# Performance work log

Hardware: AMD Instinct MI355X
Metric: run time of the kernel (lower is better)

## Reference

```python
import jax, jax.numpy as jnp
import numpy as np

V, J, NB = 6890, 52, 16
NPOSE = (J - 1) * 9  # 459 pose-blendshape features
# Standard SMPL-H kinematic tree: 22 body joints + left hand (wrist 20) + right hand (wrist 21)
PARENTS = np.array([
    -1, 0, 0, 0, 1, 2, 3, 4, 5, 6, 7, 8, 9, 9, 9, 12, 13, 14, 16, 17, 18, 19,
    20, 22, 23, 20, 25, 26, 20, 28, 29, 20, 31, 32, 20, 34, 35,
    21, 37, 38, 21, 40, 41, 21, 43, 44, 21, 46, 47, 21, 49, 50
], dtype=np.int32)


def rot6d_to_matrix(d6):
    # d6: (..., 6) -> (..., 3, 3), rows are the Gram-Schmidt basis (pytorch3d convention)
    a1, a2 = d6[..., :3], d6[..., 3:]
    b1 = a1 / jnp.linalg.norm(a1, axis=-1, keepdims=True)
    a2p = a2 - jnp.sum(b1 * a2, axis=-1, keepdims=True) * b1
    b2 = a2p / jnp.linalg.norm(a2p, axis=-1, keepdims=True)
    b3 = jnp.cross(b1, b2)
    return jnp.stack([b1, b2, b3], axis=-2)


def rigid_transform(rot_mats, joints):
    # rot_mats: (B, J, 3, 3); joints: (B, J, 3) -> relative transforms (B, J, 4, 4)
    rel = jnp.concatenate(
        [joints[..., :1, :], joints[..., 1:, :] - joints[..., PARENTS[1:], :]], axis=-2)
    tm = jnp.concatenate([rot_mats, rel[..., None]], axis=-1)  # (B, J, 3, 4)
    bottom = jnp.zeros(tm.shape[:-2] + (1, 4), dtype=tm.dtype).at[..., 0, 3].set(1.0)
    tm = jnp.concatenate([tm, bottom], axis=-2)  # (B, J, 4, 4)
    chain = [tm[..., 0, :, :]]
    for i in range(1, J):  # fixed 52-joint tree, unrolled
        chain.append(chain[int(PARENTS[i])] @ tm[..., i, :, :])
    transforms = jnp.stack(chain, axis=-3)  # (B, J, 4, 4)
    t_corr = jnp.einsum('bjcd,bjd->bjc', transforms[..., :3, :3], joints)
    return transforms.at[..., :3, 3].add(-t_corr)


def lbs_forward(body_pose, betas, global_orient, transl,
                v_template, shapedirs, posedirs, J_template, J_shapedirs, lbs_weights):
    full_pose = jnp.concatenate([global_orient, body_pose], axis=-2)  # (B, 52, 6)
    rot_mats = rot6d_to_matrix(full_pose)                              # (B, 52, 3, 3)
    joints = J_template + jnp.einsum('bk,jck->bjc', betas, J_shapedirs)
    A = rigid_transform(rot_mats, joints)                              # (B, 52, 4, 4)
    eye = jnp.eye(3, dtype=rot_mats.dtype)
    pose_feature = (rot_mats[..., 1:, :, :] - eye).reshape(rot_mats.shape[0], NPOSE)
    v_posed = (v_template
               + jnp.einsum('bk,vck->bvc', betas, shapedirs)
               + jnp.einsum('bk,kvc->bvc', pose_feature, posedirs))    # (B, V, 3)
    T = jnp.einsum('vj,bjcd->bvcd', lbs_weights, A)                    # (B, V, 4, 4)
    verts = jnp.einsum('bvcd,bvd->bvc', T[..., :3, :3], v_posed) + T[..., :3, 3]
    return verts + transl[..., None, :]


def setup_inputs() -> dict:
    key = jax.random.key(0)
    ks = jax.random.split(key, 10)
    B = 1024
    return {
        'body_pose': jax.random.normal(ks[0], (B, J - 1, 6), jnp.float32),
        'betas': jax.random.normal(ks[1], (B, NB), jnp.float32),
        'global_orient': jax.random.normal(ks[2], (B, 1, 6), jnp.float32),
        'transl': jax.random.normal(ks[3], (B, 3), jnp.float32),
        'v_template': jax.random.normal(ks[4], (V, 3), jnp.float32) * 0.3,
        'shapedirs': jax.random.normal(ks[5], (V, 3, NB), jnp.float32) * 0.01,
        'posedirs': jax.random.normal(ks[6], (NPOSE, V, 3), jnp.float32) * 0.01,
        'J_template': jax.random.normal(ks[7], (J, 3), jnp.float32) * 0.3,
        'J_shapedirs': jax.random.normal(ks[8], (J, 3, NB), jnp.float32) * 0.01,
        'lbs_weights': jax.nn.softmax(jax.random.normal(ks[9], (V, J), jnp.float32) * 2.0, axis=-1),
    }


def reference(body_pose, betas, global_orient, transl,
              v_template, shapedirs, posedirs, J_template, J_shapedirs, lbs_weights):
    return lbs_forward(body_pose, betas, global_orient, transl,
                       v_template, shapedirs, posedirs, J_template, J_shapedirs, lbs_weights)
```

## Files before the change

kernel.cpp:

```cpp
#include <hip/hip_runtime.h>

typedef unsigned short u16;
typedef __bf16  bf16x8 __attribute__((ext_vector_type(8)));
typedef float   f32x4  __attribute__((ext_vector_type(4)));
typedef unsigned int u32x4 __attribute__((ext_vector_type(4)));

#define B_SZ   1024
#define V_SZ   6890
#define VPADB  6912
#define J_SZ   52
#define NB_SZ  16
#define NPOSE  459
#define N3     20670
#define NPAD   20736
#define KG     480
#define KA     160
#define MROWS  12288

#define NK1    (B_SZ / 4)
#define NK0W   (VPADB / 64)
#define NK0    (648 * 15)

__constant__ int PARENTS_D[52] = {-1,0,0,0,1,2,3,4,5,6,7,8,9,9,9,12,13,14,16,17,18,19,20,22,23,
                                  20,25,26,20,28,29,20,31,32,20,34,35,21,37,38,21,40,41,21,43,44,
                                  21,46,47,21,49,50};

__device__ __forceinline__ u16 f2b(float f) {
  union { float f; unsigned u; } v; v.f = f;
  unsigned r = (v.u + 0x7FFFu + ((v.u >> 16) & 1u)) >> 16;
  return (u16)r;
}
__device__ __forceinline__ float b2f(u16 h) {
  union { unsigned u; float f; } v; v.u = ((unsigned)h) << 16;
  return v.f;
}
__device__ __forceinline__ void async16(const void* g, void* l) {
  __builtin_amdgcn_global_load_lds((const __attribute__((address_space(1))) void*)g,
                                   (__attribute__((address_space(3))) void*)l, 16, 0, 0);
}

__global__ __launch_bounds__(256) void k_prep(const float* __restrict__ posedirs,
                                              const float* __restrict__ shapedirs,
                                              const float* __restrict__ lbsw,
                                              const float* __restrict__ body_pose,
                                              const float* __restrict__ betas,
                                              const float* __restrict__ global_orient,
                                              const float* __restrict__ J_template,
                                              const float* __restrict__ J_shapedirs,
                                              u16* __restrict__ PDt,
                                              u16* __restrict__ WB,
                                              u16* __restrict__ AH,
                                              u16* __restrict__ PF)
{
  __shared__ __align__(16) char smem[35328];
  const int bid = blockIdx.x;
  const int tid = threadIdx.x;

  if (bid < NK1) {
    const int g = tid >> 6;
    const int t = tid & 63;
    const int b = bid * 4 + g;
    char* base = smem + g * 8832;
    float (*R)[9]   = (float(*)[9])(base);
    float (*jts)[3] = (float(*)[3])(base + 1872);
    float (*G)[12]  = (float(*)[12])(base + 2496);
    u16*   AHs      = (u16*)(base + 4992);

    for (int i = t; i < 12 * KA / 2; i += 64) ((unsigned*)AHs)[i] = 0u;

    if (t < J_SZ) {
      const float* d6 = (t == 0) ? &global_orient[(size_t)b * 6]
                                 : &body_pose[((size_t)b * 51 + (t - 1)) * 6];
      float a1x = d6[0], a1y = d6[1], a1z = d6[2];
      float a2x = d6[3], a2y = d6[4], a2z = d6[5];
      float inv1 = rsqrtf(a1x*a1x + a1y*a1y + a1z*a1z);
      float b1x = a1x*inv1, b1y = a1y*inv1, b1z = a1z*inv1;
      float d   = b1x*a2x + b1y*a2y + b1z*a2z;
      float ux = a2x - d*b1x, uy = a2y - d*b1y, uz = a2z - d*b1z;
      float inv2 = rsqrtf(ux*ux + uy*uy + uz*uz);
      float b2x = ux*inv2, b2y = uy*inv2, b2z = uz*inv2;
      float b3x = b1y*b2z - b1z*b2y;
      float b3y = b1z*b2x - b1x*b2z;
      float b3z = b1x*b2y - b1y*b2x;
      R[t][0]=b1x; R[t][1]=b1y; R[t][2]=b1z;
      R[t][3]=b2x; R[t][4]=b2y; R[t][5]=b2z;
      R[t][6]=b3x; R[t][7]=b3y; R[t][8]=b3z;
#pragma unroll
      for (int c = 0; c < 3; ++c) {
        float s = J_template[t*3 + c];
#pragma unroll
        for (int k = 0; k < NB_SZ; ++k)
          s += betas[(size_t)b*NB_SZ + k] * J_shapedirs[(t*3 + c)*NB_SZ + k];
        jts[t][c] = s;
      }
    }
    __syncthreads();

    if (t < 3) {
      const int c = t;
      G[0][c*4+0] = R[0][c*3+0];
      G[0][c*4+1] = R[0][c*3+1];
      G[0][c*4+2] = R[0][c*3+2];
      G[0][c*4+3] = jts[0][c];
      for (int j = 1; j < J_SZ; ++j) {
        int p = PARENTS_D[j];
        float r0 = jts[j][0] - jts[p][0];
        float r1 = jts[j][1] - jts[p][1];
        float r2 = jts[j][2] - jts[p][2];
        float g0 = G[p][c*4+0], g1 = G[p][c*4+1], g2 = G[p][c*4+2];
        G[j][c*4+0] = g0*R[j][0] + g1*R[j][3] + g2*R[j][6];
        G[j][c*4+1] = g0*R[j][1] + g1*R[j][4] + g2*R[j][7];
        G[j][c*4+2] = g0*R[j][2] + g1*R[j][5] + g2*R[j][8];
        G[j][c*4+3] = g0*r0 + g1*r1 + g2*r2 + G[p][c*4+3];
      }
    }
    __syncthreads();

    if (t < J_SZ) {
      float o[12];
#pragma unroll
      for (int i = 0; i < 12; ++i) o[i] = G[t][i];
#pragma unroll
      for (int c = 0; c < 3; ++c)
        o[c*4+3] -= o[c*4+0]*jts[t][0] + o[c*4+1]*jts[t][1] + o[c*4+2]*jts[t][2];
#pragma unroll
      for (int cd = 0; cd < 12; ++cd) {
        u16 hi = f2b(o[cd]);
        u16 lo = f2b(o[cd] - b2f(hi));
        AHs[cd*KA + t]        = hi;
        AHs[cd*KA + 52 + t]   = lo;
        AHs[cd*KA + 104 + t]  = hi;
      }
    }

    for (int k = t; k < KG; k += 64) {
      float val = 0.f;
      if (k < NPOSE) {
        int j  = k / 9 + 1;
        int rc = k - (j - 1) * 9;
        val = R[j][rc] - ((rc == 0 || rc == 4 || rc == 8) ? 1.f : 0.f);
      } else if (k < NPOSE + NB_SZ) {
        val = betas[(size_t)b*NB_SZ + (k - NPOSE)];
      }
      PF[(size_t)b*KG + k] = f2b(val);
    }

    __syncthreads();
    unsigned* dst = (unsigned*)(AH + (size_t)b * 12 * KA);
    for (int i = t; i < 12 * KA / 2; i += 64) dst[i] = ((const unsigned*)AHs)[i];

  } else if (bid < NK1 + NK0W) {
    u16* wtile = (u16*)smem;
    const int v0  = (bid - NK1) * 64;
    const int vl  = tid >> 2;
    const int v   = v0 + vl;
    const int jseg = (tid & 3) * 13;

    wtile[vl * KA + 156 + (tid & 3)] = 0;

#pragma unroll
    for (int jj = 0; jj < 13; ++jj) {
      int j = jseg + jj;
      float wv = (v < V_SZ) ? lbsw[(size_t)v * J_SZ + j] : 0.f;
      u16 hi = f2b(wv);
      u16 lo = f2b(wv - b2f(hi));
      wtile[vl * KA + j]        = hi;
      wtile[vl * KA + 52 + j]   = hi;
      wtile[vl * KA + 104 + j]  = lo;
    }
    __syncthreads();
    u32x4*       dst = (u32x4*)(WB + (size_t)v0 * KA);
    const u32x4* src = (const u32x4*)wtile;
    for (int i = tid; i < 64 * KA / 8; i += 256) dst[i] = src[i];

  } else {
    u16 (*tile)[33] = (u16(*)[33])smem;
    const int cb = bid - NK1 - NK0W;
    const int tx = tid & 31;
    const int ty = tid >> 5;
    const int n0 = (cb % 648) * 32;
    const int k0 = (cb / 648) * 32;
#pragma unroll
    for (int i = 0; i < 4; ++i) {
      int k = k0 + ty + i*8;
      int n = n0 + tx;
      float val = 0.f;
      if (n < N3) {
        if (k < NPOSE)              val = posedirs[(size_t)k * N3 + n];
        else if (k < NPOSE + NB_SZ) val = shapedirs[(size_t)n * NB_SZ + (k - NPOSE)];
      }
      tile[ty + i*8][tx] = f2b(val);
    }
    __syncthreads();
#pragma unroll
    for (int i = 0; i < 4; ++i) {
      int n = n0 + ty + i*8;
      int k = k0 + tx;
      int vv = n / 3;
      int cc = n - vv * 3;
      PDt[((size_t)cc * VPADB + vv) * KG + k] = tile[tx][ty + i*8];
    }
  }
}

__global__ __launch_bounds__(256) void k2_gemm(const u16* __restrict__ PF,
                                               const u16* __restrict__ PDt,
                                               const float* __restrict__ vtmpl,
                                               u16* __restrict__ VP)
{
  __shared__ __align__(16) u16 lA[2][4096];
  __shared__ __align__(16) u16 lB[2][4096];
  const int bid = blockIdx.x;
  const int nt  = (bid & 7) + ((bid >> 6) << 3);
  const int bt  = (bid >> 3) & 7;
  if (nt >= 162) return;
  const int tid  = threadIdx.x;
  const int lane = tid & 63;
  const int w    = tid >> 6;
  const int n0   = nt * 128;
  const int b0   = bt * 128;
  const int moff = (w & 1) * 64;
  const int noff = (w >> 1) * 64;
  const int q    = lane >> 4;
  const int lrow = lane & 15;

  f32x4 acc[4][4];
#pragma unroll
  for (int i = 0; i < 4; ++i)
#pragma unroll
    for (int j = 0; j < 4; ++j) { f32x4 z = {0.f,0.f,0.f,0.f}; acc[i][j] = z; }

  int aoff[4], boff[4];
#pragma unroll
  for (int i = 0; i < 4; ++i) {
    int ra = moff + i*16 + lrow;
    aoff[i] = ra*32 + (q ^ ((ra + (ra >> 2)) & 3)) * 8;
    int rb = noff + i*16 + lrow;
    boff[i] = rb*32 + (q ^ ((rb + (rb >> 2)) & 3)) * 8;
  }
  int srow[2], schunk[2];
#pragma unroll
  for (int t = 0; t < 2; ++t) {
    int i = (t*4 + w)*64 + lane;
    int r = i >> 2;
    srow[t]   = r;
    schunk[t] = (i & 3) ^ ((r + (r >> 2)) & 3);
  }

#define K2_STAGE(buf, seg)                                                          \
  {                                                                                 \
    const int kk = (seg) * 32;                                                      \
    _Pragma("unroll")                                                               \
    for (int t = 0; t < 2; ++t) {                                                   \
      async16(PF  + (size_t)(b0 + srow[t])*KG + kk + schunk[t]*8,                   \
              &lA[buf][(t*4 + w)*512]);                                             \
      async16(PDt + (size_t)(n0 + srow[t])*KG + kk + schunk[t]*8,                   \
              &lB[buf][(t*4 + w)*512]);                                             \
    }                                                                               \
  }

  K2_STAGE(0, 0);

  for (int seg = 0; seg < 15; ++seg) {
    const int cur = seg & 1;
    if (seg < 14) K2_STAGE(cur ^ 1, seg + 1);
    __builtin_amdgcn_sched_barrier(0);
    if (seg < 14) asm volatile("s_waitcnt vmcnt(4)" ::: "memory");
    else          asm volatile("s_waitcnt vmcnt(0)" ::: "memory");
    __builtin_amdgcn_s_barrier();
    __builtin_amdgcn_sched_barrier(0);
    bf16x8 af[4], bfv[4];
#pragma unroll
    for (int i = 0; i < 4; ++i) af[i]  = *(const bf16x8*)&lA[cur][aoff[i]];
#pragma unroll
    for (int i = 0; i < 4; ++i) bfv[i] = *(const bf16x8*)&lB[cur][boff[i]];
#pragma unroll
    for (int i = 0; i < 4; ++i)
#pragma unroll
      for (int j = 0; j < 4; ++j)
        acc[i][j] = __builtin_amdgcn_mfma_f32_16x16x32_bf16(af[i], bfv[j], acc[i][j], 0, 0, 0);
    if (seg < 14) {
      __builtin_amdgcn_sched_barrier(0);
      __builtin_amdgcn_s_barrier();
    }
  }
#undef K2_STAGE

#pragma unroll
  for (int i = 0; i < 4; ++i) {
    int brow = b0 + moff + i*16 + q*4;
#pragma unroll
    for (int j = 0; j < 4; ++j) {
      int np = n0 + noff + j*16 + lrow;
      int vv = np % VPADB;
      int cc = np / VPADB;
      float bias = (vv < V_SZ) ? vtmpl[vv*3 + cc] : 0.f;
#pragma unroll
      for (int r = 0; r < 4; ++r)
        VP[(size_t)(brow + r)*NPAD + np] = f2b(acc[i][j][r] + bias);
    }
  }
}

__global__ __launch_bounds__(256) void k4_blend(const u16* __restrict__ AH,
                                                const u16* __restrict__ WB,
                                                const u16* __restrict__ VP,
                                                const float* __restrict__ transl,
                                                float* __restrict__ out)
{
  __shared__ __align__(16) u16 lA[2][4096];
  __shared__ __align__(16) u16 lB[2][4096];
  const int tid  = threadIdx.x;
  const int lane = tid & 63;
  const int w    = tid >> 6;
  const int n0   = blockIdx.x * 128;
  const int m0   = blockIdx.y * 128;
  const int moff = (w & 1) * 64;
  const int noff = (w >> 1) * 64;
  const int q    = lane >> 4;
  const int lrow = lane & 15;

  int srow[2], schunk[2];
#pragma unroll
  for (int t = 0; t < 2; ++t) {
    int i = (t*4 + w)*64 + lane;
    int r = i >> 2;
    srow[t]   = r;
    schunk[t] = (i & 3) ^ ((r + (r >> 2)) & 3);
  }

#define K4_STAGE(buf, seg)                                                          \
  {                                                                                 \
    const int kk = (seg) * 32;                                                      \
    _Pragma("unroll")                                                               \
    for (int t = 0; t < 2; ++t) {                                                   \
      async16(AH + (size_t)(m0 + srow[t])*KA + kk + schunk[t]*8,                    \
              &lA[buf][(t*4 + w)*512]);                                             \
      async16(WB + (size_t)(n0 + srow[t])*KA + kk + schunk[t]*8,                    \
              &lB[buf][(t*4 + w)*512]);                                             \
    }                                                                               \
  }

  int   bp[4], cp[4];
#pragma unroll
  for (int i = 0; i < 4; ++i) {
    int gq = (m0 + moff + i*16) / 4 + q;
    bp[i] = gq / 3;
    cp[i] = gq - bp[i]*3;
  }
  u16 pv[4][4][3];
#pragma unroll
  for (int i = 0; i < 4; ++i) {
    const u16* vpb = VP + (size_t)bp[i] * NPAD;
#pragma unroll
    for (int j = 0; j < 4; ++j) {
      const int v = n0 + noff + j*16 + lrow;
      pv[i][j][0] = vpb[0*VPADB + v];
      pv[i][j][1] = vpb[1*VPADB + v];
      pv[i][j][2] = vpb[2*VPADB + v];
    }
  }
  float tr[4];
#pragma unroll
  for (int i = 0; i < 4; ++i) tr[i] = transl[bp[i]*3 + cp[i]];

  K4_STAGE(0, 0);

  f32x4 acc[4][4];
#pragma unroll
  for (int i = 0; i < 4; ++i)
#pragma unroll
    for (int j = 0; j < 4; ++j) { f32x4 z = {0.f,0.f,0.f,0.f}; acc[i][j] = z; }

  int aoff[4], boff[4];
#pragma unroll
  for (int i = 0; i < 4; ++i) {
    int ra = moff + i*16 + lrow;
    aoff[i] = ra*32 + (q ^ ((ra + (ra >> 2)) & 3)) * 8;
    int rb = noff + i*16 + lrow;
    boff[i] = rb*32 + (q ^ ((rb + (rb >> 2)) & 3)) * 8;
  }

#pragma unroll
  for (int seg = 0; seg < 5; ++seg) {
    const int cur = seg & 1;
    if (seg < 4) K4_STAGE(cur ^ 1, seg + 1);
    __builtin_amdgcn_sched_barrier(0);
    if (seg < 4) asm volatile("s_waitcnt vmcnt(4)" ::: "memory");
    else         asm volatile("s_waitcnt vmcnt(0)" ::: "memory");
    __builtin_amdgcn_s_barrier();
    __builtin_amdgcn_sched_barrier(0);
    bf16x8 af[4], bfv[4];
#pragma unroll
    for (int i = 0; i < 4; ++i) af[i]  = *(const bf16x8*)&lA[cur][aoff[i]];
#pragma unroll
    for (int i = 0; i < 4; ++i) bfv[i] = *(const bf16x8*)&lB[cur][boff[i]];
#pragma unroll
    for (int i = 0; i < 4; ++i)
#pragma unroll
      for (int j = 0; j < 4; ++j)
        acc[i][j] = __builtin_amdgcn_mfma_f32_16x16x32_bf16(af[i], bfv[j], acc[i][j], 0, 0, 0);
    if (seg < 4) {
      __builtin_amdgcn_sched_barrier(0);
      __builtin_amdgcn_s_barrier();
    }
  }
#undef K4_STAGE

#pragma unroll
  for (int i = 0; i < 4; ++i) {
    float* ob = out + (size_t)bp[i] * (V_SZ * 3);
#pragma unroll
    for (int j = 0; j < 4; ++j) {
      const int v = n0 + noff + j*16 + lrow;
      if (v < V_SZ) {
        float p0 = b2f(pv[i][j][0]);
        float p1 = b2f(pv[i][j][1]);
        float p2 = b2f(pv[i][j][2]);
        f32x4 a = acc[i][j];
        ob[(size_t)v*3 + cp[i]] = a[0]*p0 + a[1]*p1 + a[2]*p2 + a[3] + tr[i];
      }
    }
  }
}

extern "C" void kernel_launch(void* const* d_in, const int* in_sizes, int n_in,
                              void* d_out, int out_size, void* d_ws, size_t ws_size,
                              hipStream_t stream) {
  const float* body_pose     = (const float*)d_in[0];
  const float* betas         = (const float*)d_in[1];
  const float* global_orient = (const float*)d_in[2];
  const float* transl        = (const float*)d_in[3];
  const float* v_template    = (const float*)d_in[4];
  const float* shapedirs     = (const float*)d_in[5];
  const float* posedirs      = (const float*)d_in[6];
  const float* J_template    = (const float*)d_in[7];
  const float* J_shapedirs   = (const float*)d_in[8];
  const float* lbsw          = (const float*)d_in[9];
  float* out = (float*)d_out;

  char* ws = (char*)d_ws;
  u16* PF  = (u16*)(ws);
  u16* AH  = (u16*)(ws + 1048576u);
  u16* WB  = (u16*)(ws + 6291456u);
  u16* PDt = (u16*)(ws + 8503296u);
  u16* VP  = (u16*)(ws + 28409856u);

  k_prep<<<dim3(NK1 + NK0W + NK0), dim3(256), 0, stream>>>(
      posedirs, shapedirs, lbsw, body_pose, betas, global_orient,
      J_template, J_shapedirs, PDt, WB, AH, PF);
  k2_gemm<<<dim3(1344), dim3(256), 0, stream>>>(PF, PDt, v_template, VP);
  k4_blend<<<dim3(VPADB / 128, MROWS / 128), dim3(256), 0, stream>>>(AH, WB, VP, transl, out);
}
```

Measured before the change: 246.4 us.

## Enlarge blend kernel M-tile to 192 rows and stage posed vertices through LDS

```diff
diff --git a/kernel.cpp b/kernel.cpp
--- a/kernel.cpp
+++ b/kernel.cpp
@@ -16,6 +16,7 @@
 #define KG     480
 #define KA     160
 #define MROWS  12288
+#define MT     192
 
 #define NK1    (B_SZ / 4)
 #define NK0W   (VPADB / 64)
@@ -308,77 +309,79 @@
                                                 const float* __restrict__ transl,
                                                 float* __restrict__ out)
 {
-  __shared__ __align__(16) u16 lA[2][4096];
-  __shared__ __align__(16) u16 lB[2][4096];
+  __shared__ __align__(16) u16 lA[2][MT*32];
+  __shared__ __align__(16) u16 lB[2][128*32];
+  __shared__ __align__(16) u16 VPL[48*128];
   const int tid  = threadIdx.x;
   const int lane = tid & 63;
   const int w    = tid >> 6;
   const int n0   = blockIdx.x * 128;
-  const int m0   = blockIdx.y * 128;
-  const int moff = (w & 1) * 64;
-  const int noff = (w >> 1) * 64;
+  const int m0   = blockIdx.y * MT;
+  const int bfirst = blockIdx.y * 16;
+  const int mhalf = (w >> 1) * 96;
+  const int noff  = (w & 1) * 64;
   const int q    = lane >> 4;
   const int lrow = lane & 15;
 
-  int srow[2], schunk[2];
+  int srowA[3], schunkA[3];
+#pragma unroll
+  for (int t = 0; t < 3; ++t) {
+    int i = (t*4 + w)*64 + lane;
+    int r = i >> 2;
+    srowA[t]   = r;
+    schunkA[t] = (i & 3) ^ ((r + (r >> 2)) & 3);
+  }
+  int srowB[2], schunkB[2];
 #pragma unroll
   for (int t = 0; t < 2; ++t) {
     int i = (t*4 + w)*64 + lane;
     int r = i >> 2;
-    srow[t]   = r;
-    schunk[t] = (i & 3) ^ ((r + (r >> 2)) & 3);
+    srowB[t]   = r;
+    schunkB[t] = (i & 3) ^ ((r + (r >> 2)) & 3);
   }
 
 #define K4_STAGE(buf, seg)                                                          \
   {                                                                                 \
     const int kk = (seg) * 32;                                                      \
     _Pragma("unroll")                                                               \
-    for (int t = 0; t < 2; ++t) {                                                   \
-      async16(AH + (size_t)(m0 + srow[t])*KA + kk + schunk[t]*8,                    \
+    for (int t = 0; t < 3; ++t)                                                     \
+      async16(AH + (size_t)(m0 + srowA[t])*KA + kk + schunkA[t]*8,                  \
               &lA[buf][(t*4 + w)*512]);                                             \
-      async16(WB + (size_t)(n0 + srow[t])*KA + kk + schunk[t]*8,                    \
+    _Pragma("unroll")                                                               \
+    for (int t = 0; t < 2; ++t)                                                     \
+      async16(WB + (size_t)(n0 + srowB[t])*KA + kk + schunkB[t]*8,                  \
               &lB[buf][(t*4 + w)*512]);                                             \
-    }                                                                               \
-  }
-
-  int   bp[4], cp[4];
-#pragma unroll
-  for (int i = 0; i < 4; ++i) {
-    int gq = (m0 + moff + i*16) / 4 + q;
-    bp[i] = gq / 3;
-    cp[i] = gq - bp[i]*3;
-  }
-  u16 pv[4][4][3];
-#pragma unroll
-  for (int i = 0; i < 4; ++i) {
-    const u16* vpb = VP + (size_t)bp[i] * NPAD;
-#pragma unroll
-    for (int j = 0; j < 4; ++j) {
-      const int v = n0 + noff + j*16 + lrow;
-      pv[i][j][0] = vpb[0*VPADB + v];
-      pv[i][j][1] = vpb[1*VPADB + v];
-      pv[i][j][2] = vpb[2*VPADB + v];
-    }
-  }
-  float tr[4];
-#pragma unroll
-  for (int i = 0; i < 4; ++i) tr[i] = transl[bp[i]*3 + cp[i]];
+  }
+
+#pragma unroll
+  for (int t = 0; t < 3; ++t) {
+    int s   = (t*4 + w)*64 + lane;
+    int row = s >> 4;
+    int col = s & 15;
+    int bl  = row / 3;
+    int c   = row - bl*3;
+    async16(VP + (size_t)(bfirst + bl)*NPAD + (size_t)c*VPADB + n0 + col*8,
+            &VPL[(t*4 + w)*512]);
+  }
 
   K4_STAGE(0, 0);
 
-  f32x4 acc[4][4];
-#pragma unroll
-  for (int i = 0; i < 4; ++i)
+  f32x4 acc[6][4];
+#pragma unroll
+  for (int i = 0; i < 6; ++i)
 #pragma unroll
     for (int j = 0; j < 4; ++j) { f32x4 z = {0.f,0.f,0.f,0.f}; acc[i][j] = z; }
 
-  int aoff[4], boff[4];
-#pragma unroll
-  for (int i = 0; i < 4; ++i) {
-    int ra = moff + i*16 + lrow;
+  int aoff[6], boff[4];
+#pragma unroll
+  for (int i = 0; i < 6; ++i) {
+    int ra = mhalf + i*16 + lrow;
     aoff[i] = ra*32 + (q ^ ((ra + (ra >> 2)) & 3)) * 8;
-    int rb = noff + i*16 + lrow;
-    boff[i] = rb*32 + (q ^ ((rb + (rb >> 2)) & 3)) * 8;
+  }
+#pragma unroll
+  for (int j = 0; j < 4; ++j) {
+    int rb = noff + j*16 + lrow;
+    boff[j] = rb*32 + (q ^ ((rb + (rb >> 2)) & 3)) * 8;
   }
 
 #pragma unroll
@@ -386,17 +389,17 @@
     const int cur = seg & 1;
     if (seg < 4) K4_STAGE(cur ^ 1, seg + 1);
     __builtin_amdgcn_sched_barrier(0);
-    if (seg < 4) asm volatile("s_waitcnt vmcnt(4)" ::: "memory");
+    if (seg < 4) asm volatile("s_waitcnt vmcnt(5)" ::: "memory");
     else         asm volatile("s_waitcnt vmcnt(0)" ::: "memory");
     __builtin_amdgcn_s_barrier();
     __builtin_amdgcn_sched_barrier(0);
-    bf16x8 af[4], bfv[4];
-#pragma unroll
-    for (int i = 0; i < 4; ++i) af[i]  = *(const bf16x8*)&lA[cur][aoff[i]];
-#pragma unroll
-    for (int i = 0; i < 4; ++i) bfv[i] = *(const bf16x8*)&lB[cur][boff[i]];
-#pragma unroll
-    for (int i = 0; i < 4; ++i)
+    bf16x8 af[6], bfv[4];
+#pragma unroll
+    for (int i = 0; i < 6; ++i) af[i]  = *(const bf16x8*)&lA[cur][aoff[i]];
+#pragma unroll
+    for (int j = 0; j < 4; ++j) bfv[j] = *(const bf16x8*)&lB[cur][boff[j]];
+#pragma unroll
+    for (int i = 0; i < 6; ++i)
 #pragma unroll
       for (int j = 0; j < 4; ++j)
         acc[i][j] = __builtin_amdgcn_mfma_f32_16x16x32_bf16(af[i], bfv[j], acc[i][j], 0, 0, 0);
@@ -408,17 +411,23 @@
 #undef K4_STAGE
 
 #pragma unroll
-  for (int i = 0; i < 4; ++i) {
-    float* ob = out + (size_t)bp[i] * (V_SZ * 3);
+  for (int i = 0; i < 6; ++i) {
+    int gq = (m0 + mhalf + i*16) / 4 + q;
+    int bp = gq / 3;
+    int cp = gq - bp*3;
+    int bl = bp - bfirst;
+    float tr = transl[bp*3 + cp];
+    float* ob = out + (size_t)bp * (V_SZ * 3);
 #pragma unroll
     for (int j = 0; j < 4; ++j) {
-      const int v = n0 + noff + j*16 + lrow;
+      const int vv = noff + j*16 + lrow;
+      const int v  = n0 + vv;
       if (v < V_SZ) {
-        float p0 = b2f(pv[i][j][0]);
-        float p1 = b2f(pv[i][j][1]);
-        float p2 = b2f(pv[i][j][2]);
+        float p0 = b2f(VPL[(bl*3 + 0)*128 + vv]);
+        float p1 = b2f(VPL[(bl*3 + 1)*128 + vv]);
+        float p2 = b2f(VPL[(bl*3 + 2)*128 + vv]);
         f32x4 a = acc[i][j];
-        ob[(size_t)v*3 + cp[i]] = a[0]*p0 + a[1]*p1 + a[2]*p2 + a[3] + tr[i];
+        ob[(size_t)v*3 + cp] = a[0]*p0 + a[1]*p1 + a[2]*p2 + a[3] + tr;
       }
     }
   }
@@ -450,5 +459,5 @@
       posedirs, shapedirs, lbsw, body_pose, betas, global_orient,
       J_template, J_shapedirs, PDt, WB, AH, PF);
   k2_gemm<<<dim3(1344), dim3(256), 0, stream>>>(PF, PDt, v_template, VP);
-  k4_blend<<<dim3(VPADB / 128, MROWS / 128), dim3(256), 0, stream>>>(AH, WB, VP, transl, out);
-}
+  k4_blend<<<dim3(VPADB / 128, MROWS / MT), dim3(256), 0, stream>>>(AH, WB, VP, transl, out);
+}
```

Result: slower. 251.9 us (+2.2%).
